# Kernel optimization log

Measured on AMD Instinct MI355X. Metric: run time of the kernel, lower is better.

Reference implementation:

```python
import jax, jax.numpy as jnp
import numpy as np
from jax import lax

SOS_IDX = 1
EOS_IDX = 2

B, T, K = 32, 256, 128


def setup_inputs() -> dict:
    key = jax.random.key(0)
    k1, k2, k3, k4 = jax.random.split(key, 4)
    h = jax.random.normal(k1, (B, T, K), dtype=jnp.float32)
    transition = jax.random.normal(k2, (K, K), dtype=jnp.float32) * 0.1
    y = jax.random.randint(k3, (B, T), 0, K)
    lengths = jnp.maximum(jax.random.randint(k4, (B,), 1, T + 1), 1)
    mask = jnp.arange(T)[None, :] < lengths[:, None]  # [B, T] bool, contiguous prefix
    return {"h": h, "transition": transition, "y": y, "lengths": lengths, "mask": mask}


def reference(h, transition, y, lengths, mask):
    """CRF negative log-likelihood, same math as CRF.nll."""
    b, t_len, k = h.shape
    # crf_scores[b,t,i,j] = h[b,t,j] + transition[i,j]
    scores = h[:, :, None, :] + transition[None, None, :, :]  # [B,T,K,K]

    # Golden path score: score of transition prev_tag -> tag at each valid step.
    prev_y = jnp.concatenate(
        [jnp.full((b, 1), SOS_IDX, dtype=y.dtype), y[:, :-1]], axis=1
    )  # [B,T]
    gold = jnp.take_along_axis(
        jnp.take_along_axis(scores, prev_y[:, :, None, None], axis=2)[:, :, 0, :],
        y[:, :, None],
        axis=2,
    )[:, :, 0]  # [B,T]
    golden_scores = jnp.sum(jnp.where(mask, gold, jnp.zeros((), h.dtype)))

    # Forward (alpha) recurrence in log space; freeze alpha past sequence end.
    alpha0 = scores[:, 0, SOS_IDX, :]  # [B,K] (all lengths >= 1)
    scores_tbkk = jnp.swapaxes(scores, 0, 1)  # [T,B,K,K]
    mask_tb = jnp.swapaxes(mask, 0, 1)  # [T,B]

    def step(alpha, xs):
        s_t, m_t = xs  # [B,K,K], [B]
        new_alpha = jax.nn.logsumexp(s_t + alpha[:, :, None], axis=1)  # [B,K]
        return jnp.where(m_t[:, None], new_alpha, alpha), None

    alpha, _ = lax.scan(step, alpha0, (scores_tbkk[1:], mask_tb[1:]))
    Z = jnp.sum(alpha[:, EOS_IDX])
    loss = (Z - golden_scores) / b
    return loss
```

## Files before the change

kernel.cpp:

```cpp
#include <hip/hip_runtime.h>
#include <stdint.h>

#define SOS_IDX 1
#define EOS_IDX 2
#define Bb 32
#define Tt 256
#define Kk 128
#define SK 136

typedef unsigned short ushort_t;
typedef __attribute__((ext_vector_type(8))) short short8;
typedef __attribute__((ext_vector_type(4))) float float4v;

__device__ __forceinline__ ushort_t f2bf(float x) {
    union { float f; uint32_t u; } c; c.f = x;
    uint32_t u = c.u + 0x7FFFu + ((c.u >> 16) & 1u);
    return (ushort_t)(u >> 16);
}
__device__ __forceinline__ float bf2f(ushort_t s) {
    union { uint32_t u; float f; } c; c.u = ((uint32_t)s) << 16;
    return c.f;
}
__device__ __forceinline__ float bflo(uint32_t u) {
    union { uint32_t u; float f; } c; c.u = u << 16; return c.f;
}
__device__ __forceinline__ float bfhi(uint32_t u) {
    union { uint32_t u; float f; } c; c.u = u & 0xFFFF0000u; return c.f;
}
__device__ __forceinline__ uint32_t pk2bf(float a, float b) {
    union { float f; uint32_t u; } ca, cb; ca.f = a; cb.f = b;
    uint32_t ua = ca.u + 0x7FFFu + ((ca.u >> 16) & 1u);
    uint32_t ub = cb.u + 0x7FFFu + ((cb.u >> 16) & 1u);
    return __builtin_amdgcn_perm(ub, ua, 0x07060302u);
}

__global__ __launch_bounds__(256) void crf_prep(const float* __restrict__ h,
                                                const float* __restrict__ trans,
                                                ushort_t* __restrict__ EH,
                                                ushort_t* __restrict__ ETT) {
    const int tid = threadIdx.x, bid = blockIdx.x;
    if (bid < 512) {
        int base = (bid * 256 + tid) * 8;
        float4 a = *(const float4*)&h[base];
        float4 b = *(const float4*)&h[base + 4];
        uint4 o;
        o.x = pk2bf(__expf(a.x), __expf(a.y));
        o.y = pk2bf(__expf(a.z), __expf(a.w));
        o.z = pk2bf(__expf(b.x), __expf(b.y));
        o.w = pk2bf(__expf(b.z), __expf(b.w));
        *(uint4*)&EH[base] = o;
    } else {
        int idx = ((bid - 512) * 256 + tid) * 8;
        int m = idx >> 7, k0 = idx & 127;
        float e[8];
#pragma unroll
        for (int r = 0; r < 8; ++r) e[r] = __expf(trans[(k0 + r) * Kk + m]);
        uint4 o;
        o.x = pk2bf(e[0], e[1]); o.y = pk2bf(e[2], e[3]);
        o.z = pk2bf(e[4], e[5]); o.w = pk2bf(e[6], e[7]);
        *(uint4*)&ETT[idx] = o;
    }
}

__global__ __launch_bounds__(256, 4) void crf_stageA(const ushort_t* __restrict__ EH,
                                                     const ushort_t* __restrict__ ETT,
                                                     const int* __restrict__ lengths,
                                                     ushort_t* __restrict__ Qt,
                                                     float* __restrict__ Ls,
                                                     int NC, int CSPAN) {
    const int st = blockIdx.x, b = blockIdx.y, c = blockIdx.z;
    const int tid = threadIdx.x;
    const int lane = tid & 63, w = tid >> 6;
    const int c15 = lane & 15, q = lane >> 4;
    const int len = lengths[b];
    int ts = c * CSPAN; if (ts < 1) ts = 1;
    int te = (c + 1) * CSPAN; if (te > Tt) te = Tt;
    const int tE = te < len ? te : len;
    if (ts >= tE) return;
    const int nsteps = tE - ts;
    const size_t qoff = ((size_t)b * NC + c) * (Kk * Kk);
    const int nbase = st * 32;

    __shared__ __align__(16) ushort_t s_S[2][32 * SK];
    __shared__ float s_wmax[2][4];

    short8 afr[2][4];
#pragma unroll
    for (int mt = 0; mt < 2; ++mt)
#pragma unroll
        for (int kt = 0; kt < 4; ++kt)
            afr[mt][kt] = *(const short8*)&ETT[(w * 32 + mt * 16 + c15) * Kk + kt * 32 + q * 8];

#pragma unroll
    for (int j = 0; j < 2; ++j) {
        int idx = j * 256 + tid;
        int nl = idx >> 4, oct = idx & 15;
        short8 z = {0, 0, 0, 0, 0, 0, 0, 0};
        int d = nbase + nl - oct * 8;
        if (d >= 0 && d < 8) z[d] = (short)0x3F80;
        *(short8*)&s_S[0][nl * SK + oct * 8] = z;
    }

    const ushort_t* ehb = EH + ((size_t)b * Tt) * Kk;
    uint2 hp0 = *(const uint2*)&ehb[(size_t)ts * Kk + w * 32 + q * 4];
    uint2 hp1 = *(const uint2*)&ehb[(size_t)ts * Kk + w * 32 + 16 + q * 4];
    __syncthreads();

    float L = 0.0f;
    int cur = 0;
    for (int s = 0; s < nsteps; ++s) {
        uint2 e0 = hp0, e1 = hp1;
        if (s + 1 < nsteps) {
            hp0 = *(const uint2*)&ehb[(size_t)(ts + s + 1) * Kk + w * 32 + q * 4];
            hp1 = *(const uint2*)&ehb[(size_t)(ts + s + 1) * Kk + w * 32 + 16 + q * 4];
        }
        float invG = 1.0f;
        if (s > 0 && (s & 3) == 0) {
            int ms = ((s >> 2) - 1) & 1;
            float g = fmaxf(fmaxf(s_wmax[ms][0], s_wmax[ms][1]),
                            fmaxf(s_wmax[ms][2], s_wmax[ms][3]));
            invG = 1.0f / g;
            L += __logf(g);
        }
        const bool isMark = ((s & 3) == 3) || (s == nsteps - 1);

        float sc0[4], sc1[4];
        sc0[0] = bflo(e0.x) * invG; sc0[1] = bfhi(e0.x) * invG;
        sc0[2] = bflo(e0.y) * invG; sc0[3] = bfhi(e0.y) * invG;
        sc1[0] = bflo(e1.x) * invG; sc1[1] = bfhi(e1.x) * invG;
        sc1[2] = bflo(e1.y) * invG; sc1[3] = bfhi(e1.y) * invG;

        short8 bfr[2][4];
        const ushort_t* ps = s_S[cur];
#pragma unroll
        for (int nt = 0; nt < 2; ++nt)
#pragma unroll
            for (int kt = 0; kt < 4; ++kt)
                bfr[nt][kt] = *(const short8*)&ps[(nt * 16 + c15) * SK + kt * 32 + q * 8];

        float4v acc[2][2];
#pragma unroll
        for (int mt = 0; mt < 2; ++mt)
#pragma unroll
            for (int nt = 0; nt < 2; ++nt) acc[mt][nt] = (float4v){0.f, 0.f, 0.f, 0.f};
#pragma unroll
        for (int kt = 0; kt < 4; ++kt)
#pragma unroll
            for (int mt = 0; mt < 2; ++mt)
#pragma unroll
                for (int nt = 0; nt < 2; ++nt)
                    acc[mt][nt] = __builtin_amdgcn_mfma_f32_16x16x32_bf16(
                        afr[mt][kt], bfr[nt][kt], acc[mt][nt], 0, 0, 0);

        int nxt = cur ^ 1;
        ushort_t* pn = s_S[nxt];
        float lmax = 0.0f;
#pragma unroll
        for (int mt = 0; mt < 2; ++mt)
#pragma unroll
            for (int nt = 0; nt < 2; ++nt) {
                float v0 = acc[mt][nt][0] * (mt ? sc1[0] : sc0[0]);
                float v1 = acc[mt][nt][1] * (mt ? sc1[1] : sc0[1]);
                float v2 = acc[mt][nt][2] * (mt ? sc1[2] : sc0[2]);
                float v3 = acc[mt][nt][3] * (mt ? sc1[3] : sc0[3]);
                lmax = fmaxf(lmax, fmaxf(fmaxf(v0, v1), fmaxf(v2, v3)));
                uint2 u; u.x = pk2bf(v0, v1); u.y = pk2bf(v2, v3);
                *(uint2*)&pn[(nt * 16 + c15) * SK + w * 32 + mt * 16 + q * 4] = u;
            }
        if (isMark) {
#pragma unroll
            for (int o = 1; o < 64; o <<= 1) lmax = fmaxf(lmax, __shfl_xor(lmax, o));
            if (lane == 0) s_wmax[(s >> 2) & 1][w] = lmax;
        }
        __syncthreads();
        cur = nxt;
    }

    int fs = ((nsteps - 1) >> 2) & 1;
    float Gf = fmaxf(fmaxf(s_wmax[fs][0], s_wmax[fs][1]),
                     fmaxf(s_wmax[fs][2], s_wmax[fs][3]));
    float dsc = 1.0f / Gf;
    L += __logf(Gf);
    const ushort_t* pc = s_S[cur];
#pragma unroll
    for (int j = 0; j < 2; ++j) {
        int idx = j * 256 + tid;
        int n = idx & 127, o = idx >> 7;
        uint4 gv; ushort_t* gp = (ushort_t*)&gv;
#pragma unroll
        for (int r = 0; r < 8; ++r)
            gp[r] = f2bf(bf2f(pc[(o * 8 + r) * SK + n]) * dsc);
        *(uint4*)&Qt[qoff + (size_t)n * Kk + nbase + o * 8] = gv;
    }
    if (tid == 0) Ls[(((size_t)b * NC + c) << 2) + st] = L;
}

__global__ __launch_bounds__(512, 1) void crf_stageB(const float* __restrict__ h,
                                                     const float* __restrict__ trans,
                                                     const int* __restrict__ y,
                                                     const int* __restrict__ lengths,
                                                     const ushort_t* __restrict__ Qt,
                                                     const float* __restrict__ Ls,
                                                     float* __restrict__ out,
                                                     int NC, int CSPAN) {
    const int b = blockIdx.x;
    const int tid = threadIdx.x;
    const int lane = tid & 63, w = tid >> 6;
    const int n = tid >> 2, qr = tid & 3;
    const int len = lengths[b];

    __shared__ __align__(16) float vbuf[2][Kk];
    __shared__ float s_wmax[2][8];
    __shared__ float red[8];
    __shared__ float gred[4];

    if (w < 4) {
        float g = 0.0f;
        if (tid < len) {
            int yt   = y[b * Tt + tid];
            int prev = (tid == 0) ? SOS_IDX : y[b * Tt + tid - 1];
            g = h[((size_t)b * Tt + tid) * Kk + yt] + trans[prev * Kk + yt];
        }
#pragma unroll
        for (int off = 32; off > 0; off >>= 1) g += __shfl_down(g, off);
        if (lane == 0) gred[w] = g;
    }

    float a0 = h[((size_t)b * Tt) * Kk + n] + trans[SOS_IDX * Kk + n];
    float m0 = a0;
#pragma unroll
    for (int o = 1; o < 64; o <<= 1) m0 = fmaxf(m0, __shfl_xor(m0, o));
    if (lane == 0) red[w] = m0;
    __syncthreads();
    {
        float4 r0 = *(const float4*)&red[0];
        float4 r1 = *(const float4*)&red[4];
        m0 = fmaxf(fmaxf(fmaxf(r0.x, r0.y), fmaxf(r0.z, r0.w)),
                   fmaxf(fmaxf(r1.x, r1.y), fmaxf(r1.z, r1.w)));
    }
    float cacc = m0;
    if (qr == 0) vbuf[0][n] = __expf(a0 - m0);

    const int NCR = (len <= 1) ? 0 : min(NC, (len + CSPAN - 1) / CSPAN);
    const size_t lbase = (size_t)b * NC;
    uint4 qb[4];
    if (NCR > 0) {
        const uint4* qp = (const uint4*)(Qt + lbase * (Kk * Kk) + n * Kk + qr * 32);
#pragma unroll
        for (int r = 0; r < 4; ++r) qb[r] = qp[r];
    }
    __syncthreads();
    if (tid == 0)
        atomicAdd(out, -(gred[0] + gred[1] + gred[2] + gred[3]) * (1.0f / (float)Bb));

    int cur = 0;
    for (int ci = 0; ci < NCR; ++ci) {
        uint4 qn[4];
        if (ci + 1 < NCR) {
            const uint4* qp2 = (const uint4*)(Qt + (lbase + ci + 1) * (Kk * Kk) + n * Kk + qr * 32);
#pragma unroll
            for (int r = 0; r < 4; ++r) qn[r] = qp2[r];
        }
        float4 Ls4 = *(const float4*)&Ls[(lbase + ci) << 2];
        float Lref = fmaxf(fmaxf(Ls4.x, Ls4.y), fmaxf(Ls4.z, Ls4.w));
        float lsq = (qr == 0) ? Ls4.x : (qr == 1) ? Ls4.y : (qr == 2) ? Ls4.z : Ls4.w;
        float eQ = __expf(lsq - Lref);
        float invG = 1.0f;
        if (ci > 0 && (ci & 3) == 0) {
            int ms = ((ci >> 2) - 1) & 1;
            float4 r0 = *(const float4*)&s_wmax[ms][0];
            float4 r1 = *(const float4*)&s_wmax[ms][4];
            float g = fmaxf(fmaxf(fmaxf(r0.x, r0.y), fmaxf(r0.z, r0.w)),
                            fmaxf(fmaxf(r1.x, r1.y), fmaxf(r1.z, r1.w)));
            invG = 1.0f / g;
            cacc += __logf(g);
        }
        cacc += Lref;

        float acc0 = 0.0f, acc1 = 0.0f;
#pragma unroll
        for (int r = 0; r < 4; ++r) {
            uint4 d = qb[r];
            float4 v0 = *(const float4*)&vbuf[cur][qr * 32 + r * 8];
            float4 v1 = *(const float4*)&vbuf[cur][qr * 32 + r * 8 + 4];
            acc0 = fmaf(bflo(d.x), v0.x, acc0);
            acc1 = fmaf(bfhi(d.x), v0.y, acc1);
            acc0 = fmaf(bflo(d.y), v0.z, acc0);
            acc1 = fmaf(bfhi(d.y), v0.w, acc1);
            acc0 = fmaf(bflo(d.z), v1.x, acc0);
            acc1 = fmaf(bfhi(d.z), v1.y, acc1);
            acc0 = fmaf(bflo(d.w), v1.z, acc0);
            acc1 = fmaf(bfhi(d.w), v1.w, acc1);
        }
        float s = (acc0 + acc1) * (eQ * invG);
        s += __shfl_xor(s, 1);
        s += __shfl_xor(s, 2);

        const bool isMark = ((ci & 3) == 3) || (ci == NCR - 1);
        if (isMark) {
            float wm = s;
#pragma unroll
            for (int o = 1; o < 64; o <<= 1) wm = fmaxf(wm, __shfl_xor(wm, o));
            if (lane == 0) s_wmax[(ci >> 2) & 1][w] = wm;
        }
        int nxt = cur ^ 1;
        if (qr == 0) vbuf[nxt][n] = s;
        __syncthreads();
        cur = nxt;
        if (ci + 1 < NCR) {
#pragma unroll
            for (int r = 0; r < 4; ++r) qb[r] = qn[r];
        }
    }

    if (tid == 0) {
        atomicAdd(out, (cacc + __logf(vbuf[cur][EOS_IDX])) * (1.0f / (float)Bb));
    }
}

extern "C" void kernel_launch(void* const* d_in, const int* in_sizes, int n_in,
                              void* d_out, int out_size, void* d_ws, size_t ws_size,
                              hipStream_t stream) {
    const float* h       = (const float*)d_in[0];
    const float* trans   = (const float*)d_in[1];
    const int*   y       = (const int*)d_in[2];
    const int*   lengths = (const int*)d_in[3];
    float* out = (float*)d_out;

    const size_t ehBytes  = (size_t)Bb * Tt * Kk * 2;
    const size_t ettBytes = (size_t)Kk * Kk * 2;
    int NC = 32;
    while (NC > 8) {
        size_t need = (size_t)Bb * NC * Kk * Kk * 2 + ehBytes + ettBytes
                    + (size_t)Bb * NC * 16;
        if (need <= ws_size) break;
        NC >>= 1;
    }
    int CSPAN = Tt / NC;
    ushort_t* Qt  = (ushort_t*)d_ws;
    ushort_t* EH  = (ushort_t*)((char*)d_ws + (size_t)Bb * NC * Kk * Kk * 2);
    ushort_t* ETT = EH + (size_t)Bb * Tt * Kk;
    float*    Ls  = (float*)(ETT + Kk * Kk);

    hipMemsetAsync(out, 0, sizeof(float), stream);
    crf_prep<<<520, 256, 0, stream>>>(h, trans, EH, ETT);
    crf_stageA<<<dim3(4, Bb, NC), 256, 0, stream>>>(EH, ETT, lengths, Qt, Ls, NC, CSPAN);
    crf_stageB<<<Bb, 512, 0, stream>>>(h, trans, y, lengths, Qt, Ls, out, NC, CSPAN);
}
```

Baseline: 130.8 us.

## Fuse exp(h) into chunk kernel and seed chunk state with first step

The prep kernel no longer converts all of h to bf16 exp values. Each chunk block now computes exp(h) for its own time steps straight into shared memory. The chunk state is initialised with the first step's transition-times-emission matrix, built from a new exp(transition) buffer, instead of an identity, which saves one matmul step per chunk. The chunk length is fixed at 16 (NC=16) rather than chosen from workspace size. This removes a full global round trip of the EH tensor and one prep pass, at the cost of redundant exp work across the 4 column blocks and more shared memory per block.

```diff
diff --git a/kernel.cpp b/kernel.cpp
--- a/kernel.cpp
+++ b/kernel.cpp
@@ -7,6 +7,7 @@
 #define Tt 256
 #define Kk 128
 #define SK 136
+#define CSP 16
 
 typedef unsigned short ushort_t;
 typedef __attribute__((ext_vector_type(8))) short short8;
@@ -34,47 +35,46 @@
     return __builtin_amdgcn_perm(ub, ua, 0x07060302u);
 }
 
-__global__ __launch_bounds__(256) void crf_prep(const float* __restrict__ h,
-                                                const float* __restrict__ trans,
-                                                ushort_t* __restrict__ EH,
-                                                ushort_t* __restrict__ ETT) {
+__global__ __launch_bounds__(256) void crf_prep(const float* __restrict__ trans,
+                                                ushort_t* __restrict__ ETT,
+                                                ushort_t* __restrict__ ET) {
     const int tid = threadIdx.x, bid = blockIdx.x;
-    if (bid < 512) {
-        int base = (bid * 256 + tid) * 8;
-        float4 a = *(const float4*)&h[base];
-        float4 b = *(const float4*)&h[base + 4];
+    int idx = ((bid & 7) * 256 + tid) * 8;
+    if (bid < 8) {
+        int m = idx >> 7, k0 = idx & 127;
+        float e[8];
+#pragma unroll
+        for (int r = 0; r < 8; ++r) e[r] = __expf(trans[(k0 + r) * Kk + m]);
+        uint4 o;
+        o.x = pk2bf(e[0], e[1]); o.y = pk2bf(e[2], e[3]);
+        o.z = pk2bf(e[4], e[5]); o.w = pk2bf(e[6], e[7]);
+        *(uint4*)&ETT[idx] = o;
+    } else {
+        float4 a = *(const float4*)&trans[idx];
+        float4 b = *(const float4*)&trans[idx + 4];
         uint4 o;
         o.x = pk2bf(__expf(a.x), __expf(a.y));
         o.y = pk2bf(__expf(a.z), __expf(a.w));
         o.z = pk2bf(__expf(b.x), __expf(b.y));
         o.w = pk2bf(__expf(b.z), __expf(b.w));
-        *(uint4*)&EH[base] = o;
-    } else {
-        int idx = ((bid - 512) * 256 + tid) * 8;
-        int m = idx >> 7, k0 = idx & 127;
-        float e[8];
-#pragma unroll
-        for (int r = 0; r < 8; ++r) e[r] = __expf(trans[(k0 + r) * Kk + m]);
-        uint4 o;
-        o.x = pk2bf(e[0], e[1]); o.y = pk2bf(e[2], e[3]);
-        o.z = pk2bf(e[4], e[5]); o.w = pk2bf(e[6], e[7]);
-        *(uint4*)&ETT[idx] = o;
-    }
-}
-
-__global__ __launch_bounds__(256, 4) void crf_stageA(const ushort_t* __restrict__ EH,
+        *(uint4*)&ET[idx] = o;
+    }
+}
+
+__global__ __launch_bounds__(256, 4) void crf_stageA(const float* __restrict__ h,
                                                      const ushort_t* __restrict__ ETT,
+                                                     const ushort_t* __restrict__ ET,
                                                      const int* __restrict__ lengths,
                                                      ushort_t* __restrict__ Qt,
                                                      float* __restrict__ Ls,
-                                                     int NC, int CSPAN) {
+                                                     int NC) {
     const int st = blockIdx.x, b = blockIdx.y, c = blockIdx.z;
     const int tid = threadIdx.x;
     const int lane = tid & 63, w = tid >> 6;
     const int c15 = lane & 15, q = lane >> 4;
     const int len = lengths[b];
-    int ts = c * CSPAN; if (ts < 1) ts = 1;
-    int te = (c + 1) * CSPAN; if (te > Tt) te = Tt;
+    int ts = c * CSP; if (ts < 1) ts = 1;
+    int te = (c + 1) * CSP; if (te > Tt) te = Tt;
     const int tE = te < len ? te : len;
     if (ts >= tE) return;
     const int nsteps = tE - ts;
@@ -82,7 +82,14 @@
     const int nbase = st * 32;
 
     __shared__ __align__(16) ushort_t s_S[2][32 * SK];
+    __shared__ __align__(16) float    s_eh[CSP][Kk];
     __shared__ float s_wmax[2][4];
+
+    for (int tl = w; tl < nsteps; tl += 4) {
+        const float* hr = &h[((size_t)b * Tt + ts + tl) * Kk];
+        s_eh[tl][lane]      = __expf(hr[lane]);
+        s_eh[tl][lane + 64] = __expf(hr[lane + 64]);
+    }
 
     short8 afr[2][4];
 #pragma unroll
@@ -90,32 +97,39 @@
 #pragma unroll
         for (int kt = 0; kt < 4; ++kt)
             afr[mt][kt] = *(const short8*)&ETT[(w * 32 + mt * 16 + c15) * Kk + kt * 32 + q * 8];
-
-#pragma unroll
-    for (int j = 0; j < 2; ++j) {
-        int idx = j * 256 + tid;
-        int nl = idx >> 4, oct = idx & 15;
-        short8 z = {0, 0, 0, 0, 0, 0, 0, 0};
-        int d = nbase + nl - oct * 8;
-        if (d >= 0 && d < 8) z[d] = (short)0x3F80;
-        *(short8*)&s_S[0][nl * SK + oct * 8] = z;
-    }
-
-    const ushort_t* ehb = EH + ((size_t)b * Tt) * Kk;
-    uint2 hp0 = *(const uint2*)&ehb[(size_t)ts * Kk + w * 32 + q * 4];
-    uint2 hp1 = *(const uint2*)&ehb[(size_t)ts * Kk + w * 32 + 16 + q * 4];
+    __syncthreads();
+
+    {
+        float lmax = 0.0f;
+#pragma unroll
+        for (int j = 0; j < 2; ++j) {
+            int idx = j * 256 + tid;
+            int nl = idx >> 4, k8 = (idx & 15) * 8;
+            uint4 ev = *(const uint4*)&ET[(nbase + nl) * Kk + k8];
+            float4 e0 = *(const float4*)&s_eh[0][k8];
+            float4 e1 = *(const float4*)&s_eh[0][k8 + 4];
+            float v0 = bflo(ev.x) * e0.x, v1 = bfhi(ev.x) * e0.y;
+            float v2 = bflo(ev.y) * e0.z, v3 = bfhi(ev.y) * e0.w;
+            float v4 = bflo(ev.z) * e1.x, v5 = bfhi(ev.z) * e1.y;
+            float v6 = bflo(ev.w) * e1.z, v7 = bfhi(ev.w) * e1.w;
+            lmax = fmaxf(lmax, fmaxf(fmaxf(fmaxf(v0, v1), fmaxf(v2, v3)),
+                                     fmaxf(fmaxf(v4, v5), fmaxf(v6, v7))));
+            uint4 o;
+            o.x = pk2bf(v0, v1); o.y = pk2bf(v2, v3);
+            o.z = pk2bf(v4, v5); o.w = pk2bf(v6, v7);
+            *(uint4*)&s_S[0][nl * SK + k8] = o;
+        }
+#pragma unroll
+        for (int o = 1; o < 64; o <<= 1) lmax = fmaxf(lmax, __shfl_xor(lmax, o));
+        if (lane == 0) s_wmax[0][w] = lmax;
+    }
     __syncthreads();
 
     float L = 0.0f;
     int cur = 0;
-    for (int s = 0; s < nsteps; ++s) {
-        uint2 e0 = hp0, e1 = hp1;
-        if (s + 1 < nsteps) {
-            hp0 = *(const uint2*)&ehb[(size_t)(ts + s + 1) * Kk + w * 32 + q * 4];
-            hp1 = *(const uint2*)&ehb[(size_t)(ts + s + 1) * Kk + w * 32 + 16 + q * 4];
-        }
+    for (int s = 1; s < nsteps; ++s) {
         float invG = 1.0f;
-        if (s > 0 && (s & 3) == 0) {
+        if ((s & 3) == 0) {
             int ms = ((s >> 2) - 1) & 1;
             float g = fmaxf(fmaxf(s_wmax[ms][0], s_wmax[ms][1]),
                             fmaxf(s_wmax[ms][2], s_wmax[ms][3]));
@@ -125,10 +139,14 @@
         const bool isMark = ((s & 3) == 3) || (s == nsteps - 1);
 
         float sc0[4], sc1[4];
-        sc0[0] = bflo(e0.x) * invG; sc0[1] = bfhi(e0.x) * invG;
-        sc0[2] = bflo(e0.y) * invG; sc0[3] = bfhi(e0.y) * invG;
-        sc1[0] = bflo(e1.x) * invG; sc1[1] = bfhi(e1.x) * invG;
-        sc1[2] = bflo(e1.y) * invG; sc1[3] = bfhi(e1.y) * invG;
+        {
+            float4 e0 = *(const float4*)&s_eh[s][w * 32 + q * 4];
+            float4 e1 = *(const float4*)&s_eh[s][w * 32 + 16 + q * 4];
+            sc0[0] = e0.x * invG; sc0[1] = e0.y * invG;
+            sc0[2] = e0.z * invG; sc0[3] = e0.w * invG;
+            sc1[0] = e1.x * invG; sc1[1] = e1.y * invG;
+            sc1[2] = e1.z * invG; sc1[3] = e1.w * invG;
+        }
 
         short8 bfr[2][4];
         const ushort_t* ps = s_S[cur];
@@ -202,7 +220,7 @@
                                                      const ushort_t* __restrict__ Qt,
                                                      const float* __restrict__ Ls,
                                                      float* __restrict__ out,
-                                                     int NC, int CSPAN) {
+                                                     int NC) {
     const int b = blockIdx.x;
     const int tid = threadIdx.x;
     const int lane = tid & 63, w = tid >> 6;
@@ -241,7 +259,7 @@
     float cacc = m0;
     if (qr == 0) vbuf[0][n] = __expf(a0 - m0);
 
-    const int NCR = (len <= 1) ? 0 : min(NC, (len + CSPAN - 1) / CSPAN);
+    const int NCR = (len <= 1) ? 0 : min(NC, (len + CSP - 1) / CSP);
     const size_t lbase = (size_t)b * NC;
     uint4 qb[4];
     if (NCR > 0) {
@@ -327,23 +345,14 @@
     const int*   lengths = (const int*)d_in[3];
     float* out = (float*)d_out;
 
-    const size_t ehBytes  = (size_t)Bb * Tt * Kk * 2;
-    const size_t ettBytes = (size_t)Kk * Kk * 2;
-    int NC = 32;
-    while (NC > 8) {
-        size_t need = (size_t)Bb * NC * Kk * Kk * 2 + ehBytes + ettBytes
-                    + (size_t)Bb * NC * 16;
-        if (need <= ws_size) break;
-        NC >>= 1;
-    }
-    int CSPAN = Tt / NC;
+    const int NC = Tt / CSP;
     ushort_t* Qt  = (ushort_t*)d_ws;
-    ushort_t* EH  = (ushort_t*)((char*)d_ws + (size_t)Bb * NC * Kk * Kk * 2);
-    ushort_t* ETT = EH + (size_t)Bb * Tt * Kk;
-    float*    Ls  = (float*)(ETT + Kk * Kk);
+    ushort_t* ETT = Qt + (size_t)Bb * NC * Kk * Kk;
+    ushort_t* ET  = ETT + Kk * Kk;
+    float*    Ls  = (float*)(ET + Kk * Kk);
 
     hipMemsetAsync(out, 0, sizeof(float), stream);
-    crf_prep<<<520, 256, 0, stream>>>(h, trans, EH, ETT);
-    crf_stageA<<<dim3(4, Bb, NC), 256, 0, stream>>>(EH, ETT, lengths, Qt, Ls, NC, CSPAN);
-    crf_stageB<<<Bb, 512, 0, stream>>>(h, trans, y, lengths, Qt, Ls, out, NC, CSPAN);
-}
+    crf_prep<<<16, 256, 0, stream>>>(trans, ETT, ET);
+    crf_stageA<<<dim3(4, Bb, NC), 256, 0, stream>>>(h, ETT, ET, lengths, Qt, Ls, NC);
+    crf_stageB<<<Bb, 512, 0, stream>>>(h, trans, y, lengths, Qt, Ls, out, NC);
+}
```

Measured after the change: 113.4 us. 13.3% less time.
